# Kernel tuning notes

Hardware: AMD Instinct MI355X
Metric: run time of the kernel (lower is better)

## Reference

```python
import jax, jax.numpy as jnp
import numpy as np

H = 32        # num_attention_heads
KVH = 8       # num_key_value_heads
D = 64        # attention_head_size
WIN = 256     # attention_window_size (left/right)
ROPE_BASE = 10000.0


def setup_inputs() -> dict:
    key = jax.random.key(0)
    k1, k2, k3 = jax.random.split(key, 3)
    B, S = 2, 2048
    return {
        "query_states": jax.random.normal(k1, (B, S, H * D), dtype=jnp.float32),
        "key_states": jax.random.normal(k2, (B, S, KVH * D), dtype=jnp.float32),
        "value_states": jax.random.normal(k3, (B, S, KVH * D), dtype=jnp.float32),
    }


def _rope_cos_sin(seq_len, dtype):
    inv_freq = 1.0 / (ROPE_BASE ** (jnp.arange(0, D, 2, dtype=jnp.float32) / D))  # [D/2]
    pos = jnp.arange(seq_len, dtype=jnp.float32)
    freqs = pos[:, None] * inv_freq[None, :]          # [S, D/2]
    emb = jnp.concatenate([freqs, freqs], axis=-1)    # [S, D]
    return jnp.cos(emb).astype(dtype), jnp.sin(emb).astype(dtype)


def _rotate_half(x):
    x1, x2 = x[..., : D // 2], x[..., D // 2 :]
    return jnp.concatenate([-x2, x1], axis=-1)


def reference(query_states, key_states, value_states):
    B, S, _ = query_states.shape
    n_rep = H // KVH

    q = query_states.reshape(B, S, H, D).transpose(0, 2, 1, 3)        # [B,H,S,D]
    k = key_states.reshape(B, S, KVH, D).transpose(0, 2, 1, 3)        # [B,KVH,S,D]
    v = value_states.reshape(B, S, KVH, D).transpose(0, 2, 1, 3)

    # repeat_kv: [B,KVH,S,D] -> [B,H,S,D]
    k = jnp.repeat(k, n_rep, axis=1)
    v = jnp.repeat(v, n_rep, axis=1)

    cos, sin = _rope_cos_sin(S, q.dtype)   # [S,D]
    cos = cos[None, None]                  # [1,1,S,D]
    sin = sin[None, None]
    q = q * cos + _rotate_half(q) * sin
    k = k * cos + _rotate_half(k) * sin

    scale = 1.0 / jnp.sqrt(jnp.asarray(D, dtype=q.dtype))
    scores = jnp.einsum("bhqd,bhkd->bhqk", q, k) * scale              # [B,H,S,S]

    i = jnp.arange(S)[:, None]
    j = jnp.arange(S)[None, :]
    allowed = (j >= i - WIN) & (j <= i)                               # [S,S]
    scores = jnp.where(allowed[None, None], scores, jnp.finfo(scores.dtype).min)

    probs = jax.nn.softmax(scores, axis=-1)
    out = jnp.einsum("bhqk,bhkd->bhqd", probs, v)                     # [B,H,S,D]
    return out.transpose(0, 2, 1, 3).reshape(B, S, H * D)
```

## Files before the change

### kernel.cpp

```cpp
#include <hip/hip_runtime.h>
#include <math.h>

#define NH   32
#define NKVH 8
#define HD   64
#define WIN  256
#define BB   2
#define SS   2048

typedef short short8 __attribute__((ext_vector_type(8)));
typedef float f32x4  __attribute__((ext_vector_type(4)));

__device__ __forceinline__ ushort f2bf(float x) {
    union { float f; unsigned u; } v; v.f = x;
    unsigned u = v.u + 0x7FFF + ((v.u >> 16) & 1);
    return (ushort)(u >> 16);
}

__device__ __forceinline__ int cvtpk_bf16(float lo, float hi) {
    int r;
    asm("v_cvt_pk_bf16_f32 %0, %1, %2" : "=v"(r) : "v"(lo), "v"(hi));
    return r;
}

__global__ __launch_bounds__(256) void prep_kv(const float* __restrict__ K,
                                               const float* __restrict__ V,
                                               ushort* __restrict__ Kr,
                                               ushort* __restrict__ Vt) {
    __shared__ ushort tile[32][65];
    const int bidx = blockIdx.x;
    const int sblk = bidx & 63;
    const int s0   = sblk * 32;
    const int kvh  = (bidx >> 6) & 7;
    const int b    = bidx >> 9;
    const int d = threadIdx.x & 63, g = threadIdx.x >> 6;

    const float inv = __powf(10000.f, -(float)(d & 31) * (1.f / 32.f));

    float kv[8], vv[8];
#pragma unroll
    for (int i = 0; i < 8; ++i) {
        int s = s0 + g * 8 + i;
        kv[i] = K[(size_t)(b * SS + s) * (NKVH * HD) + kvh * HD + d];
        vv[i] = V[(size_t)(b * SS + s) * (NKVH * HD) + kvh * HD + d];
    }
#pragma unroll
    for (int i = 0; i < 8; ++i) {
        int s  = s0 + g * 8 + i;
        int sl = g * 8 + i;
        float partner = __shfl(kv[i], d ^ 32, 64);
        float sn, cs;
        __sincosf((float)s * inv, &sn, &cs);
        float krot = kv[i] * cs + ((d < 32) ? -partner : partner) * sn;
        Kr[((size_t)(b * NKVH + kvh) * SS + s) * HD + d] = f2bf(krot);
        tile[sl][d] = f2bf(vv[i]);
    }
    __syncthreads();
    ushort* vb = Vt + (size_t)(b * NKVH + kvh) * HD * SS + (size_t)sblk * (HD * 32);
    const int sl = threadIdx.x & 31, drg = threadIdx.x >> 5;
#pragma unroll
    for (int i = 0; i < 8; ++i) {
        int dr = drg * 8 + i;
        vb[dr * 32 + sl] = tile[sl][dr];
    }
}

__global__ __launch_bounds__(256, 3) void attn_mfma(const float* __restrict__ Q,
                                                    const ushort* __restrict__ Kr,
                                                    const ushort* __restrict__ Vt,
                                                    float* __restrict__ O) {
    const int wv = threadIdx.x >> 6, lane = threadIdx.x & 63;
    const int lo16 = lane & 15, quad = lane >> 4;
    const int bidx = (blockIdx.x & 7) * 128 + (blockIdx.x >> 3);
    const int qblk = bidx & 63;
    const int kvh  = (bidx >> 6) & 7;
    const int b    = bidx >> 9;
    const int h    = kvh * 4 + wv;
    const int q0   = qblk * 32;

    float invf[8];
#pragma unroll
    for (int j = 0; j < 8; ++j)
        invf[j] = __powf(10000.f, -(float)(quad * 8 + j) * (1.f / 32.f));

    short8 aq[2][2];
#pragma unroll
    for (int t = 0; t < 2; ++t) {
        int qi = q0 + t * 16 + lo16;
        const float* qrow = Q + (size_t)(b * SS + qi) * (NH * HD) + h * HD;
        float lo[8], hi[8];
        *(float4*)(lo)     = *(const float4*)(qrow + quad * 8);
        *(float4*)(lo + 4) = *(const float4*)(qrow + quad * 8 + 4);
        *(float4*)(hi)     = *(const float4*)(qrow + 32 + quad * 8);
        *(float4*)(hi + 4) = *(const float4*)(qrow + 32 + quad * 8 + 4);
#pragma unroll
        for (int j = 0; j < 8; ++j) {
            float sn, cs;
            __sincosf((float)qi * invf[j], &sn, &cs);
            aq[t][0][j] = (short)f2bf((lo[j] * cs - hi[j] * sn) * 0.125f);
            aq[t][1][j] = (short)f2bf((hi[j] * cs + lo[j] * sn) * 0.125f);
        }
    }

    const ushort* kbase = Kr + (size_t)(b * NKVH + kvh) * SS * HD;
    const ushort* vbase = Vt + (size_t)(b * NKVH + kvh) * HD * SS;

    f32x4 acc[2][4];
#pragma unroll
    for (int t = 0; t < 2; ++t)
#pragma unroll
        for (int i = 0; i < 4; ++i) acc[t][i] = (f32x4){0.f, 0.f, 0.f, 0.f};
    float psum[2] = {0.f, 0.f};

    const int idxAB = (lo16 + ((quad & 1) << 5)) << 2;
    const int idxCD = idxAB + 64;
    const bool hiq  = quad >= 2;

    int klo = q0 - WIN; if (klo < 0) klo = 0;
    const int khi = q0 + 31;

    short8 kcur[4], vcur[4];
    {
        int key0 = klo + lo16, key1 = klo + 16 + lo16;
        kcur[0] = *(const short8*)(kbase + (size_t)key0 * HD + quad * 8);
        kcur[1] = *(const short8*)(kbase + (size_t)key0 * HD + 32 + quad * 8);
        kcur[2] = *(const short8*)(kbase + (size_t)key1 * HD + quad * 8);
        kcur[3] = *(const short8*)(kbase + (size_t)key1 * HD + 32 + quad * 8);
        int cidx = klo >> 5;
#pragma unroll
        for (int i = 0; i < 4; ++i)
            vcur[i] = *(const short8*)(vbase + (size_t)cidx * (HD * 32)
                                             + (i * 16 + lo16) * 32 + quad * 8);
    }

    for (int kb = klo; kb <= khi; kb += 32) {
        const f32x4 z = {0.f, 0.f, 0.f, 0.f};
        __builtin_amdgcn_s_setprio(1);
        f32x4 s00 = __builtin_amdgcn_mfma_f32_16x16x32_bf16(kcur[0], aq[0][0], z,   0, 0, 0);
        s00       = __builtin_amdgcn_mfma_f32_16x16x32_bf16(kcur[1], aq[0][1], s00, 0, 0, 0);
        f32x4 s01 = __builtin_amdgcn_mfma_f32_16x16x32_bf16(kcur[2], aq[0][0], z,   0, 0, 0);
        s01       = __builtin_amdgcn_mfma_f32_16x16x32_bf16(kcur[3], aq[0][1], s01, 0, 0, 0);
        f32x4 s10 = __builtin_amdgcn_mfma_f32_16x16x32_bf16(kcur[0], aq[1][0], z,   0, 0, 0);
        s10       = __builtin_amdgcn_mfma_f32_16x16x32_bf16(kcur[1], aq[1][1], s10, 0, 0, 0);
        f32x4 s11 = __builtin_amdgcn_mfma_f32_16x16x32_bf16(kcur[2], aq[1][0], z,   0, 0, 0);
        s11       = __builtin_amdgcn_mfma_f32_16x16x32_bf16(kcur[3], aq[1][1], s11, 0, 0, 0);
        __builtin_amdgcn_s_setprio(0);

        short8 knxt[4], vnxt[4];
        {
            int key0 = kb + 32 + lo16; if (key0 > SS - 1) key0 = SS - 1;
            int key1 = key0 + 16;      if (key1 > SS - 1) key1 = SS - 1;
            knxt[0] = *(const short8*)(kbase + (size_t)key0 * HD + quad * 8);
            knxt[1] = *(const short8*)(kbase + (size_t)key0 * HD + 32 + quad * 8);
            knxt[2] = *(const short8*)(kbase + (size_t)key1 * HD + quad * 8);
            knxt[3] = *(const short8*)(kbase + (size_t)key1 * HD + 32 + quad * 8);
            int cnx = (kb >> 5) + 1; if (cnx > (SS / 32) - 1) cnx = (SS / 32) - 1;
#pragma unroll
            for (int i = 0; i < 4; ++i)
                vnxt[i] = *(const short8*)(vbase + (size_t)cnx * (HD * 32)
                                                 + (i * 16 + lo16) * 32 + quad * 8);
        }

        short8 ap[2];
#pragma unroll
        for (int t = 0; t < 2; ++t) {
            const f32x4 sa = t ? s10 : s00;
            const f32x4 sb = t ? s11 : s01;
            const int qtmin = q0 + t * 16;
            const int myq   = qtmin + lo16;
            float p[8];
            if ((kb + 31 > qtmin) || (kb < qtmin + 15 - WIN)) {
#pragma unroll
                for (int r = 0; r < 4; ++r) {
                    int key0 = kb + quad * 4 + r;
                    int key1 = key0 + 16;
                    p[r]     = (key0 <= myq && key0 >= myq - WIN) ? __expf(sa[r]) : 0.f;
                    p[4 + r] = (key1 <= myq && key1 >= myq - WIN) ? __expf(sb[r]) : 0.f;
                }
            } else {
#pragma unroll
                for (int r = 0; r < 4; ++r) { p[r] = __expf(sa[r]); p[4 + r] = __expf(sb[r]); }
            }
            psum[t] += ((p[0] + p[1]) + (p[2] + p[3])) + ((p[4] + p[5]) + (p[6] + p[7]));

            int w0 = cvtpk_bf16(p[0], p[1]);
            int w1 = cvtpk_bf16(p[2], p[3]);
            int w2 = cvtpk_bf16(p[4], p[5]);
            int w3 = cvtpk_bf16(p[6], p[7]);
            int a0 = __builtin_amdgcn_ds_bpermute(idxAB, w0);
            int a2 = __builtin_amdgcn_ds_bpermute(idxAB, w2);
            int b1 = __builtin_amdgcn_ds_bpermute(idxAB, w1);
            int b3 = __builtin_amdgcn_ds_bpermute(idxAB, w3);
            int c0 = __builtin_amdgcn_ds_bpermute(idxCD, w0);
            int c2 = __builtin_amdgcn_ds_bpermute(idxCD, w2);
            int d1 = __builtin_amdgcn_ds_bpermute(idxCD, w1);
            int d3 = __builtin_amdgcn_ds_bpermute(idxCD, w3);
            union { int i[4]; short8 s; } u;
            u.i[0] = hiq ? a2 : a0;
            u.i[1] = hiq ? b3 : b1;
            u.i[2] = hiq ? c2 : c0;
            u.i[3] = hiq ? d3 : d1;
            ap[t] = u.s;
        }

        __builtin_amdgcn_s_setprio(1);
#pragma unroll
        for (int i = 0; i < 4; ++i)
            acc[0][i] = __builtin_amdgcn_mfma_f32_16x16x32_bf16(ap[0], vcur[i], acc[0][i], 0, 0, 0);
#pragma unroll
        for (int i = 0; i < 4; ++i)
            acc[1][i] = __builtin_amdgcn_mfma_f32_16x16x32_bf16(ap[1], vcur[i], acc[1][i], 0, 0, 0);
        __builtin_amdgcn_s_setprio(0);

#pragma unroll
        for (int i = 0; i < 4; ++i) { kcur[i] = knxt[i]; vcur[i] = vnxt[i]; }
    }

#pragma unroll
    for (int t = 0; t < 2; ++t) {
        float ps = psum[t];
        ps += __shfl_xor(ps, 16, 64);
        ps += __shfl_xor(ps, 32, 64);
#pragma unroll
        for (int r = 0; r < 4; ++r) {
            float invr = 1.f / __shfl(ps, quad * 4 + r, 16);
            int qr = q0 + t * 16 + quad * 4 + r;
            size_t orow = ((size_t)(b * SS + qr) * NH + h) * HD;
            O[orow + 0 * 16 + lo16] = acc[t][0][r] * invr;
            O[orow + 1 * 16 + lo16] = acc[t][1][r] * invr;
            O[orow + 2 * 16 + lo16] = acc[t][2][r] * invr;
            O[orow + 3 * 16 + lo16] = acc[t][3][r] * invr;
        }
    }
}

__device__ __forceinline__ float wave_sum(float x) {
#pragma unroll
    for (int off = 32; off > 0; off >>= 1) x += __shfl_xor(x, off, 64);
    return x;
}

__global__ __launch_bounds__(256) void attn_scalar(const float* __restrict__ Q,
                                                   const float* __restrict__ K,
                                                   const float* __restrict__ V,
                                                   float* __restrict__ O) {
    int wave = blockIdx.x * 4 + (threadIdx.x >> 6);
    int lane = threadIdx.x & 63;
    int q  = wave % SS;
    int bh = wave / SS;
    int h  = bh % NH;
    int b  = bh / NH;
    int kvh = h >> 2;

    float inv = __powf(10000.f, -(float)(lane & 31) * (1.f / 32.f));
    float sn, cs;
    __sincosf((float)q * inv, &sn, &cs);

    float qv = Q[(size_t)(b * SS + q) * (NH * HD) + h * HD + lane];
    float qpart = __shfl(qv, lane ^ 32, 64);
    float qrot = (qv * cs + ((lane < 32) ? -qpart : qpart) * sn) * 0.125f;

    const float* vbase = V + (size_t)b * SS * (NKVH * HD) + kvh * HD;
    float m = -1e30f, l = 0.f, acc = 0.f;
    int k0 = q - WIN; if (k0 < 0) k0 = 0;
    for (int k = k0; k <= q; ++k) {
        float kraw = K[(size_t)(b * SS + k) * (NKVH * HD) + kvh * HD + lane];
        float kpart = __shfl(kraw, lane ^ 32, 64);
        float ksn, kcs;
        __sincosf((float)k * inv, &ksn, &kcs);
        float kv = kraw * kcs + ((lane < 32) ? -kpart : kpart) * ksn;
        float vv = vbase[(size_t)k * (NKVH * HD) + lane];
        float score = wave_sum(qrot * kv);
        float mnew  = fmaxf(m, score);
        float alpha = __expf(m - mnew);
        float p     = __expf(score - mnew);
        l   = l * alpha + p;
        acc = acc * alpha + p * vv;
        m   = mnew;
    }
    O[(((size_t)(b * SS + q) * NH) + h) * HD + lane] = acc / l;
}

extern "C" void kernel_launch(void* const* d_in, const int* in_sizes, int n_in,
                              void* d_out, int out_size, void* d_ws, size_t ws_size,
                              hipStream_t stream) {
    const float* Q = (const float*)d_in[0];
    const float* K = (const float*)d_in[1];
    const float* V = (const float*)d_in[2];
    float* O = (float*)d_out;

    size_t kv_elems = (size_t)BB * NKVH * SS * HD;
    size_t need = 2 * kv_elems * sizeof(ushort);

    if (ws_size >= need) {
        ushort* Kr = (ushort*)d_ws;
        ushort* Vt = Kr + kv_elems;
        prep_kv<<<BB * NKVH * (SS / 32), 256, 0, stream>>>(K, V, Kr, Vt);
        attn_mfma<<<BB * NKVH * (SS / 32), 256, 0, stream>>>(Q, Kr, Vt, O);
    } else {
        attn_scalar<<<(BB * NH * SS) / 4, 256, 0, stream>>>(Q, K, V, O);
    }
}
```

Baseline: 134.8 us.

## Split key range across two waves per head and combine partials in LDS

The attention kernel now gives each block a single head and query tile, with two waves each covering half of the key-block range. Wave 1 writes its partial output accumulators and row sums to shared memory, and wave 0 adds them in before normalising and writing the result. This quadruples the grid and roughly halves each wave's serial loop, to improve latency hiding and occupancy. The cost is the LDS reduction and a block barrier, and the four heads sharing a KV head no longer share one block, so K/V reuse now depends on the cache. The V-transpose store in the prep kernel is also widened to two elements per write.

```diff
diff --git a/kernel.cpp b/kernel.cpp
--- a/kernel.cpp
+++ b/kernel.cpp
@@ -57,25 +57,29 @@
     }
     __syncthreads();
     ushort* vb = Vt + (size_t)(b * NKVH + kvh) * HD * SS + (size_t)sblk * (HD * 32);
-    const int sl = threadIdx.x & 31, drg = threadIdx.x >> 5;
-#pragma unroll
-    for (int i = 0; i < 8; ++i) {
-        int dr = drg * 8 + i;
-        vb[dr * 32 + sl] = tile[sl][dr];
-    }
-}
-
-__global__ __launch_bounds__(256, 3) void attn_mfma(const float* __restrict__ Q,
-                                                    const ushort* __restrict__ Kr,
-                                                    const ushort* __restrict__ Vt,
-                                                    float* __restrict__ O) {
+    const int sl2 = (threadIdx.x & 15) * 2, drg = threadIdx.x >> 4;
+#pragma unroll
+    for (int i = 0; i < 4; ++i) {
+        int dr = drg * 4 + i;
+        ushort2 u = make_ushort2(tile[sl2][dr], tile[sl2 + 1][dr]);
+        *(ushort2*)(vb + dr * 32 + sl2) = u;
+    }
+}
+
+__global__ __launch_bounds__(128) void attn_mfma(const float* __restrict__ Q,
+                                                 const ushort* __restrict__ Kr,
+                                                 const ushort* __restrict__ Vt,
+                                                 float* __restrict__ O) {
+    __shared__ float cbuf[32][65];
+    __shared__ float csum[32];
     const int wv = threadIdx.x >> 6, lane = threadIdx.x & 63;
     const int lo16 = lane & 15, quad = lane >> 4;
-    const int bidx = (blockIdx.x & 7) * 128 + (blockIdx.x >> 3);
-    const int qblk = bidx & 63;
-    const int kvh  = (bidx >> 6) & 7;
-    const int b    = bidx >> 9;
-    const int h    = kvh * 4 + wv;
+    const int bidx = (blockIdx.x & 7) * 512 + (blockIdx.x >> 3);
+    const int h2   = bidx & 3;
+    const int qblk = (bidx >> 2) & 63;
+    const int kvh  = (bidx >> 8) & 7;
+    const int b    = bidx >> 11;
+    const int h    = kvh * 4 + h2;
     const int q0   = qblk * 32;
 
     float invf[8];
@@ -118,22 +122,27 @@
 
     int klo = q0 - WIN; if (klo < 0) klo = 0;
     const int khi = q0 + 31;
+    const int n   = (khi - klo + 32) >> 5;
+    const int n0  = (n + 1) >> 1;
+    const int cnt = wv ? (n - n0) : n0;
+    const int kb0 = klo + (wv ? n0 * 32 : 0);
 
     short8 kcur[4], vcur[4];
     {
-        int key0 = klo + lo16, key1 = klo + 16 + lo16;
+        int key0 = kb0 + lo16, key1 = kb0 + 16 + lo16;
         kcur[0] = *(const short8*)(kbase + (size_t)key0 * HD + quad * 8);
         kcur[1] = *(const short8*)(kbase + (size_t)key0 * HD + 32 + quad * 8);
         kcur[2] = *(const short8*)(kbase + (size_t)key1 * HD + quad * 8);
         kcur[3] = *(const short8*)(kbase + (size_t)key1 * HD + 32 + quad * 8);
-        int cidx = klo >> 5;
+        int cidx = kb0 >> 5;
 #pragma unroll
         for (int i = 0; i < 4; ++i)
             vcur[i] = *(const short8*)(vbase + (size_t)cidx * (HD * 32)
                                              + (i * 16 + lo16) * 32 + quad * 8);
     }
 
-    for (int kb = klo; kb <= khi; kb += 32) {
+    for (int it = 0; it < cnt; ++it) {
+        const int kb = kb0 + it * 32;
         const f32x4 z = {0.f, 0.f, 0.f, 0.f};
         __builtin_amdgcn_s_setprio(1);
         f32x4 s00 = __builtin_amdgcn_mfma_f32_16x16x32_bf16(kcur[0], aq[0][0], z,   0, 0, 0);
@@ -216,20 +225,51 @@
         for (int i = 0; i < 4; ++i) { kcur[i] = knxt[i]; vcur[i] = vnxt[i]; }
     }
 
+    float pst[2];
 #pragma unroll
     for (int t = 0; t < 2; ++t) {
         float ps = psum[t];
         ps += __shfl_xor(ps, 16, 64);
         ps += __shfl_xor(ps, 32, 64);
-#pragma unroll
-        for (int r = 0; r < 4; ++r) {
-            float invr = 1.f / __shfl(ps, quad * 4 + r, 16);
-            int qr = q0 + t * 16 + quad * 4 + r;
-            size_t orow = ((size_t)(b * SS + qr) * NH + h) * HD;
-            O[orow + 0 * 16 + lo16] = acc[t][0][r] * invr;
-            O[orow + 1 * 16 + lo16] = acc[t][1][r] * invr;
-            O[orow + 2 * 16 + lo16] = acc[t][2][r] * invr;
-            O[orow + 3 * 16 + lo16] = acc[t][3][r] * invr;
+        pst[t] = ps;
+    }
+    if (wv == 1) {
+#pragma unroll
+        for (int t = 0; t < 2; ++t)
+#pragma unroll
+            for (int r = 0; r < 4; ++r) {
+                int q = t * 16 + quad * 4 + r;
+#pragma unroll
+                for (int i = 0; i < 4; ++i)
+                    cbuf[q][i * 16 + lo16] = acc[t][i][r];
+            }
+        if (quad == 0) { csum[lo16] = pst[0]; csum[16 + lo16] = pst[1]; }
+    }
+    __syncthreads();
+    if (wv == 0) {
+        pst[0] += csum[lo16];
+        pst[1] += csum[16 + lo16];
+#pragma unroll
+        for (int t = 0; t < 2; ++t)
+#pragma unroll
+            for (int r = 0; r < 4; ++r) {
+                int q = t * 16 + quad * 4 + r;
+#pragma unroll
+                for (int i = 0; i < 4; ++i)
+                    acc[t][i][r] += cbuf[q][i * 16 + lo16];
+            }
+#pragma unroll
+        for (int t = 0; t < 2; ++t) {
+#pragma unroll
+            for (int r = 0; r < 4; ++r) {
+                float invr = 1.f / __shfl(pst[t], quad * 4 + r, 16);
+                int qr = q0 + t * 16 + quad * 4 + r;
+                size_t orow = ((size_t)(b * SS + qr) * NH + h) * HD;
+                O[orow + 0 * 16 + lo16] = acc[t][0][r] * invr;
+                O[orow + 1 * 16 + lo16] = acc[t][1][r] * invr;
+                O[orow + 2 * 16 + lo16] = acc[t][2][r] * invr;
+                O[orow + 3 * 16 + lo16] = acc[t][3][r] * invr;
+            }
         }
     }
 }
@@ -296,7 +336,7 @@
         ushort* Kr = (ushort*)d_ws;
         ushort* Vt = Kr + kv_elems;
         prep_kv<<<BB * NKVH * (SS / 32), 256, 0, stream>>>(K, V, Kr, Vt);
-        attn_mfma<<<BB * NKVH * (SS / 32), 256, 0, stream>>>(Q, Kr, Vt, O);
+        attn_mfma<<<BB * NKVH * (SS / 32) * 4, 128, 0, stream>>>(Q, Kr, Vt, O);
     } else {
         attn_scalar<<<(BB * NH * SS) / 4, 256, 0, stream>>>(Q, K, V, O);
     }
```

After: 136.0 us. Within noise of the previous version (+0.9%).

## Stage K/V tiles into swizzled LDS via direct global-to-LDS double buffering

Applied to the files above, without the earlier changes.

The prep kernel now writes K and V in an XOR-swizzled 4KB-per-chunk layout. The attention kernel stages each 32-key K and V chunk into double-buffered LDS with global_load_lds and has the four waves, one per head of the GQA group, share it instead of each loading its own copy into registers. This cuts redundant global/L2 traffic by four and frees registers, so launch bounds go up to 4 blocks per CU. The cost is a __syncthreads per iteration, and the prefetch wait relies on that barrier for ordering.

```diff
diff --git a/kernel.cpp b/kernel.cpp
--- a/kernel.cpp
+++ b/kernel.cpp
@@ -21,6 +21,14 @@
     int r;
     asm("v_cvt_pk_bf16_f32 %0, %1, %2" : "=v"(r) : "v"(lo), "v"(hi));
     return r;
+}
+
+__device__ __forceinline__ int swz(int L) { return L ^ (((L >> 7) & 7) << 4); }
+
+__device__ __forceinline__ void stage16(const void* g, void* l) {
+    __builtin_amdgcn_global_load_lds(
+        (const __attribute__((address_space(1))) unsigned int*)g,
+        (__attribute__((address_space(3))) unsigned int*)l, 16, 0, 0);
 }
 
 __global__ __launch_bounds__(256) void prep_kv(const float* __restrict__ K,
@@ -44,6 +52,7 @@
         kv[i] = K[(size_t)(b * SS + s) * (NKVH * HD) + kvh * HD + d];
         vv[i] = V[(size_t)(b * SS + s) * (NKVH * HD) + kvh * HD + d];
     }
+    char* kc = (char*)(Kr + (size_t)(b * NKVH + kvh) * SS * HD) + (size_t)sblk * 4096;
 #pragma unroll
     for (int i = 0; i < 8; ++i) {
         int s  = s0 + g * 8 + i;
@@ -52,23 +61,26 @@
         float sn, cs;
         __sincosf((float)s * inv, &sn, &cs);
         float krot = kv[i] * cs + ((d < 32) ? -partner : partner) * sn;
-        Kr[((size_t)(b * NKVH + kvh) * SS + s) * HD + d] = f2bf(krot);
+        *(ushort*)(kc + swz(sl * 128 + d * 2)) = f2bf(krot);
         tile[sl][d] = f2bf(vv[i]);
     }
     __syncthreads();
-    ushort* vb = Vt + (size_t)(b * NKVH + kvh) * HD * SS + (size_t)sblk * (HD * 32);
-    const int sl = threadIdx.x & 31, drg = threadIdx.x >> 5;
-#pragma unroll
-    for (int i = 0; i < 8; ++i) {
-        int dr = drg * 8 + i;
-        vb[dr * 32 + sl] = tile[sl][dr];
-    }
-}
-
-__global__ __launch_bounds__(256, 3) void attn_mfma(const float* __restrict__ Q,
+    char* vc = (char*)(Vt + (size_t)(b * NKVH + kvh) * HD * SS) + (size_t)sblk * 4096;
+    const int sl2 = (threadIdx.x & 15) * 2, drg = threadIdx.x >> 4;
+#pragma unroll
+    for (int i = 0; i < 4; ++i) {
+        int dr = drg * 4 + i;
+        ushort2 u = make_ushort2(tile[sl2][dr], tile[sl2 + 1][dr]);
+        *(ushort2*)(vc + swz(dr * 64 + sl2 * 2)) = u;
+    }
+}
+
+__global__ __launch_bounds__(256, 4) void attn_mfma(const float* __restrict__ Q,
                                                     const ushort* __restrict__ Kr,
                                                     const ushort* __restrict__ Vt,
                                                     float* __restrict__ O) {
+    __shared__ __align__(16) ushort ldsK[2][2048];
+    __shared__ __align__(16) ushort ldsV[2][2048];
     const int wv = threadIdx.x >> 6, lane = threadIdx.x & 63;
     const int lo16 = lane & 15, quad = lane >> 4;
     const int bidx = (blockIdx.x & 7) * 128 + (blockIdx.x >> 3);
@@ -102,8 +114,8 @@
         }
     }
 
-    const ushort* kbase = Kr + (size_t)(b * NKVH + kvh) * SS * HD;
-    const ushort* vbase = Vt + (size_t)(b * NKVH + kvh) * HD * SS;
+    const char* kbase = (const char*)(Kr + (size_t)(b * NKVH + kvh) * SS * HD);
+    const char* vbase = (const char*)(Vt + (size_t)(b * NKVH + kvh) * HD * SS);
 
     f32x4 acc[2][4];
 #pragma unroll
@@ -117,49 +129,44 @@
     const bool hiq  = quad >= 2;
 
     int klo = q0 - WIN; if (klo < 0) klo = 0;
-    const int khi = q0 + 31;
-
-    short8 kcur[4], vcur[4];
+    const int c0  = klo >> 5;
+    const int cnt = (q0 >> 5) - c0 + 1;
+
     {
-        int key0 = klo + lo16, key1 = klo + 16 + lo16;
-        kcur[0] = *(const short8*)(kbase + (size_t)key0 * HD + quad * 8);
-        kcur[1] = *(const short8*)(kbase + (size_t)key0 * HD + 32 + quad * 8);
-        kcur[2] = *(const short8*)(kbase + (size_t)key1 * HD + quad * 8);
-        kcur[3] = *(const short8*)(kbase + (size_t)key1 * HD + 32 + quad * 8);
-        int cidx = klo >> 5;
-#pragma unroll
-        for (int i = 0; i < 4; ++i)
-            vcur[i] = *(const short8*)(vbase + (size_t)cidx * (HD * 32)
-                                             + (i * 16 + lo16) * 32 + quad * 8);
-    }
-
-    for (int kb = klo; kb <= khi; kb += 32) {
+        const char* kc = kbase + (size_t)c0 * 4096 + wv * 1024 + lane * 16;
+        const char* vc = vbase + (size_t)c0 * 4096 + wv * 1024 + lane * 16;
+        stage16(kc, (char*)&ldsK[0][0] + wv * 1024);
+        stage16(vc, (char*)&ldsV[0][0] + wv * 1024);
+    }
+    __syncthreads();
+
+    int nb = 0;
+    for (int it = 0; it < cnt; ++it, nb ^= 1) {
+        const int kb = klo + it * 32;
+        if (it + 1 < cnt) {
+            const char* kc = kbase + (size_t)(c0 + it + 1) * 4096 + wv * 1024 + lane * 16;
+            const char* vc = vbase + (size_t)(c0 + it + 1) * 4096 + wv * 1024 + lane * 16;
+            stage16(kc, (char*)&ldsK[nb ^ 1][0] + wv * 1024);
+            stage16(vc, (char*)&ldsV[nb ^ 1][0] + wv * 1024);
+        }
+
+        const char* kl = (const char*)&ldsK[nb][0];
+        short8 k0 = *(const short8*)(kl + swz(lo16 * 128 + quad * 16));
+        short8 k1 = *(const short8*)(kl + swz(lo16 * 128 + 64 + quad * 16));
+        short8 k2 = *(const short8*)(kl + swz((lo16 + 16) * 128 + quad * 16));
+        short8 k3 = *(const short8*)(kl + swz((lo16 + 16) * 128 + 64 + quad * 16));
+
         const f32x4 z = {0.f, 0.f, 0.f, 0.f};
         __builtin_amdgcn_s_setprio(1);
-        f32x4 s00 = __builtin_amdgcn_mfma_f32_16x16x32_bf16(kcur[0], aq[0][0], z,   0, 0, 0);
-        s00       = __builtin_amdgcn_mfma_f32_16x16x32_bf16(kcur[1], aq[0][1], s00, 0, 0, 0);
-        f32x4 s01 = __builtin_amdgcn_mfma_f32_16x16x32_bf16(kcur[2], aq[0][0], z,   0, 0, 0);
-        s01       = __builtin_amdgcn_mfma_f32_16x16x32_bf16(kcur[3], aq[0][1], s01, 0, 0, 0);
-        f32x4 s10 = __builtin_amdgcn_mfma_f32_16x16x32_bf16(kcur[0], aq[1][0], z,   0, 0, 0);
-        s10       = __builtin_amdgcn_mfma_f32_16x16x32_bf16(kcur[1], aq[1][1], s10, 0, 0, 0);
-        f32x4 s11 = __builtin_amdgcn_mfma_f32_16x16x32_bf16(kcur[2], aq[1][0], z,   0, 0, 0);
-        s11       = __builtin_amdgcn_mfma_f32_16x16x32_bf16(kcur[3], aq[1][1], s11, 0, 0, 0);
+        f32x4 s00 = __builtin_amdgcn_mfma_f32_16x16x32_bf16(k0, aq[0][0], z,   0, 0, 0);
+        s00       = __builtin_amdgcn_mfma_f32_16x16x32_bf16(k1, aq[0][1], s00, 0, 0, 0);
+        f32x4 s01 = __builtin_amdgcn_mfma_f32_16x16x32_bf16(k2, aq[0][0], z,   0, 0, 0);
+        s01       = __builtin_amdgcn_mfma_f32_16x16x32_bf16(k3, aq[0][1], s01, 0, 0, 0);
+        f32x4 s10 = __builtin_amdgcn_mfma_f32_16x16x32_bf16(k0, aq[1][0], z,   0, 0, 0);
+        s10       = __builtin_amdgcn_mfma_f32_16x16x32_bf16(k1, aq[1][1], s10, 0, 0, 0);
+        f32x4 s11 = __builtin_amdgcn_mfma_f32_16x16x32_bf16(k2, aq[1][0], z,   0, 0, 0);
+        s11       = __builtin_amdgcn_mfma_f32_16x16x32_bf16(k3, aq[1][1], s11, 0, 0, 0);
         __builtin_amdgcn_s_setprio(0);
-
-        short8 knxt[4], vnxt[4];
-        {
-            int key0 = kb + 32 + lo16; if (key0 > SS - 1) key0 = SS - 1;
-            int key1 = key0 + 16;      if (key1 > SS - 1) key1 = SS - 1;
-            knxt[0] = *(const short8*)(kbase + (size_t)key0 * HD + quad * 8);
-            knxt[1] = *(const short8*)(kbase + (size_t)key0 * HD + 32 + quad * 8);
-            knxt[2] = *(const short8*)(kbase + (size_t)key1 * HD + quad * 8);
-            knxt[3] = *(const short8*)(kbase + (size_t)key1 * HD + 32 + quad * 8);
-            int cnx = (kb >> 5) + 1; if (cnx > (SS / 32) - 1) cnx = (SS / 32) - 1;
-#pragma unroll
-            for (int i = 0; i < 4; ++i)
-                vnxt[i] = *(const short8*)(vbase + (size_t)cnx * (HD * 32)
-                                                 + (i * 16 + lo16) * 32 + quad * 8);
-        }
 
         short8 ap[2];
 #pragma unroll
@@ -191,29 +198,34 @@
             int a2 = __builtin_amdgcn_ds_bpermute(idxAB, w2);
             int b1 = __builtin_amdgcn_ds_bpermute(idxAB, w1);
             int b3 = __builtin_amdgcn_ds_bpermute(idxAB, w3);
-            int c0 = __builtin_amdgcn_ds_bpermute(idxCD, w0);
-            int c2 = __builtin_amdgcn_ds_bpermute(idxCD, w2);
+            int cc0 = __builtin_amdgcn_ds_bpermute(idxCD, w0);
+            int cc2 = __builtin_amdgcn_ds_bpermute(idxCD, w2);
             int d1 = __builtin_amdgcn_ds_bpermute(idxCD, w1);
             int d3 = __builtin_amdgcn_ds_bpermute(idxCD, w3);
             union { int i[4]; short8 s; } u;
-            u.i[0] = hiq ? a2 : a0;
-            u.i[1] = hiq ? b3 : b1;
-            u.i[2] = hiq ? c2 : c0;
-            u.i[3] = hiq ? d3 : d1;
+            u.i[0] = hiq ? a2  : a0;
+            u.i[1] = hiq ? b3  : b1;
+            u.i[2] = hiq ? cc2 : cc0;
+            u.i[3] = hiq ? d3  : d1;
             ap[t] = u.s;
         }
 
+        const char* vl = (const char*)&ldsV[nb][0];
+        short8 vf[4];
+#pragma unroll
+        for (int i = 0; i < 4; ++i)
+            vf[i] = *(const short8*)(vl + swz((i * 16 + lo16) * 64 + quad * 16));
+
         __builtin_amdgcn_s_setprio(1);
 #pragma unroll
         for (int i = 0; i < 4; ++i)
-            acc[0][i] = __builtin_amdgcn_mfma_f32_16x16x32_bf16(ap[0], vcur[i], acc[0][i], 0, 0, 0);
+            acc[0][i] = __builtin_amdgcn_mfma_f32_16x16x32_bf16(ap[0], vf[i], acc[0][i], 0, 0, 0);
 #pragma unroll
         for (int i = 0; i < 4; ++i)
-            acc[1][i] = __builtin_amdgcn_mfma_f32_16x16x32_bf16(ap[1], vcur[i], acc[1][i], 0, 0, 0);
+            acc[1][i] = __builtin_amdgcn_mfma_f32_16x16x32_bf16(ap[1], vf[i], acc[1][i], 0, 0, 0);
         __builtin_amdgcn_s_setprio(0);
 
-#pragma unroll
-        for (int i = 0; i < 4; ++i) { kcur[i] = knxt[i]; vcur[i] = vnxt[i]; }
+        __syncthreads();
     }
 
 #pragma unroll
```

After: 114.8 us. 1.17x faster.
